# Optimization experiments

Hardware: AMD Instinct MI355X
Metric: run time of the kernel (lower is better)

The kernel has to match this reference:

```python
import jax, jax.numpy as jnp
import numpy as np

BLOCK = 8
NUM_BINS = 64

def _make_dct_basis(n):
    i = np.arange(n)[:, None].astype(np.float64)
    j = np.arange(n)[None, :].astype(np.float64)
    scale = np.where(i == 0, np.sqrt(1.0 / n), np.sqrt(2.0 / n))
    basis = scale * np.cos(np.pi * i * (2.0 * j + 1.0) / (2.0 * n))
    return jnp.asarray(basis, dtype=jnp.float32)

def setup_inputs() -> dict:
    key = jax.random.key(0)
    x = jax.random.normal(key, (32, 3, 512, 512), dtype=jnp.float32)
    return {"x": x, "dct_basis": _make_dct_basis(BLOCK)}

def reference(x, dct_basis):
    B, C, H, W = x.shape
    bs = BLOCK
    # H, W assumed multiples of bs (pad branch is a no-op for these shapes)
    # tile into non-overlapping bs x bs blocks: [B, C, n_blocks, bs, bs]
    blocks = x.reshape(B, C, H // bs, bs, W // bs, bs)
    blocks = blocks.transpose(0, 1, 2, 4, 3, 5).reshape(B, C, -1, bs, bs)
    # 2D block DCT: D @ block @ D^T
    dct = jnp.einsum('ij,bcnjk,kl->bcnil', dct_basis, blocks, dct_basis)
    # flatten coeffs per block, drop DC coefficient
    flat = dct.reshape(B, C, -1, bs * bs)[..., 1:]
    mag = jnp.abs(flat)
    hist_max = jnp.max(mag) * 1.1  # global max, matches torch code
    # torch.histc semantics: uniform bins on [0, hist_max], edge value -> last bin
    bin_idx = jnp.floor(mag * (NUM_BINS / hist_max)).astype(jnp.int32)
    bin_idx = jnp.clip(bin_idx, 0, NUM_BINS - 1)
    # fused per-(b, c) histogram via a single segment_sum
    bc = jnp.arange(B)[:, None] * C + jnp.arange(C)[None, :]  # [B, C]
    seg = (bc[:, :, None, None] * NUM_BINS + bin_idx).reshape(-1)
    counts = jax.ops.segment_sum(
        jnp.ones(seg.shape, dtype=x.dtype), seg, num_segments=B * C * NUM_BINS)
    hists = counts.reshape(B, C * NUM_BINS) / (H * W)
    return hists
```

## Files before the change

### kernel.cpp

```cpp
#include <hip/hip_runtime.h>


#define NUM_BINS 64
#define HREP 16
#define NWG1 1536
#define MAGS_OFF 8192

typedef unsigned int uint;
typedef __fp16 fp16x2 __attribute__((ext_vector_type(2)));

__device__ __forceinline__ void load_block(const float* __restrict__ p, float* blk) {
    #pragma unroll
    for (int r = 0; r < 8; ++r) {
        float4 a = *reinterpret_cast<const float4*>(p + (size_t)r * 512);
        float4 b = *reinterpret_cast<const float4*>(p + (size_t)r * 512 + 4);
        blk[r*8+0]=a.x; blk[r*8+1]=a.y; blk[r*8+2]=a.z; blk[r*8+3]=a.w;
        blk[r*8+4]=b.x; blk[r*8+5]=b.y; blk[r*8+6]=b.z; blk[r*8+7]=b.w;
    }
}

template <typename F>
__device__ __forceinline__ float dct_block_sym(const float* Dh, float* blk, F&& emit) {
    #pragma unroll
    for (int j = 0; j < 4; ++j)
        #pragma unroll
        for (int k = 0; k < 8; ++k) {
            float a = blk[j*8+k], b = blk[(7-j)*8+k];
            blk[j*8+k]     = a + b;
            blk[(7-j)*8+k] = a - b;
        }

    float m = 0.0f;
    #pragma unroll
    for (int i = 0; i < 8; ++i) {
        float u[8];
        #pragma unroll
        for (int k = 0; k < 8; ++k) {
            float s = 0.0f;
            #pragma unroll
            for (int j = 0; j < 4; ++j) {
                int row = (i & 1) ? (7 - j) : j;
                s = fmaf(Dh[i*4+j], blk[row*8+k], s);
            }
            u[k] = s;
        }
        #pragma unroll
        for (int l = 0; l < 4; ++l) {
            float e = 0.0f, o = 0.0f;
            #pragma unroll
            for (int k = 0; k < 4; ++k) {
                e = fmaf(u[2*k],   Dh[(2*k)*4+l],   e);
                o = fmaf(u[2*k+1], Dh[(2*k+1)*4+l], o);
            }
            float v0 = e + o;
            float v1 = e - o;
            float m1 = fabsf(v1);
            m = fmaxf(m, m1);
            emit(m1);
            if (i != 0 || l != 0) {
                float m0 = fabsf(v0);
                m = fmaxf(m, m0);
                emit(m0);
            }
        }
    }
    return m;
}

struct NoEmit { __device__ void operator()(float) const {} };

template <bool WRITE_MAGS>
__global__ __launch_bounds__(256) void dct_max_kernel(
    const float* __restrict__ x, const float* __restrict__ basis,
    float* __restrict__ wgmax, uint* __restrict__ mags, float* __restrict__ out)
{
    __shared__ float wred[4];
    float Dh[32];
    #pragma unroll
    for (int r = 0; r < 8; ++r)
        #pragma unroll
        for (int c = 0; c < 4; ++c)
            Dh[r*4+c] = basis[r*8+c];

    if (blockIdx.x < 24) out[blockIdx.x * 256 + threadIdx.x] = 0.0f;

    int tid = blockIdx.x * 256 + threadIdx.x;
    int bc  = tid >> 12;
    int n   = tid & 4095;
    int hb  = n >> 6, wb = n & 63;
    const float* p = x + ((size_t)bc << 18) + ((size_t)(hb * 8) << 9) + (size_t)(wb * 8);

    float blk[64];
    load_block(p, blk);

    float m;
    if (WRITE_MAGS) {
        uint* wbase = mags + (size_t)(tid >> 6) * 2048 + (tid & 63);
        float flo = 0.0f;
        int   e   = 0;
        m = dct_block_sym(Dh, blk, [&](float mag) {
            if ((e & 1) == 0) {
                flo = mag;
            } else {
                fp16x2 h2 = __builtin_amdgcn_cvt_pkrtz(flo, mag);
                wbase[(e >> 1) * 64] = __builtin_bit_cast(uint, h2);
            }
            ++e;
        });
        fp16x2 h2 = __builtin_amdgcn_cvt_pkrtz(flo, -__builtin_inff());
        wbase[31 * 64] = __builtin_bit_cast(uint, h2);
    } else {
        m = dct_block_sym(Dh, blk, NoEmit{});
    }

    #pragma unroll
    for (int off = 32; off > 0; off >>= 1)
        m = fmaxf(m, __shfl_down(m, off, 64));
    if ((threadIdx.x & 63) == 0) wred[threadIdx.x >> 6] = m;
    __syncthreads();
    if (threadIdx.x == 0)
        wgmax[blockIdx.x] = fmaxf(fmaxf(wred[0], wred[1]), fmaxf(wred[2], wred[3]));
}

__device__ __forceinline__ float reduce_scale(const float* __restrict__ wgmax,
                                              float* wred, float* s_scale) {
    float m = 0.0f;
    for (int i = threadIdx.x; i < NWG1; i += 256) m = fmaxf(m, wgmax[i]);
    #pragma unroll
    for (int off = 32; off > 0; off >>= 1)
        m = fmaxf(m, __shfl_down(m, off, 64));
    if ((threadIdx.x & 63) == 0) wred[threadIdx.x >> 6] = m;
    __syncthreads();
    if (threadIdx.x == 0) {
        float mm = fmaxf(fmaxf(wred[0], wred[1]), fmaxf(wred[2], wred[3]));
        *s_scale = (float)NUM_BINS / (mm * 1.1f);
    }
    __syncthreads();
    return *s_scale;
}

__global__ __launch_bounds__(256) void dct_hist_frommags(
    const uint* __restrict__ mags, const float* __restrict__ wgmax,
    float* __restrict__ out)
{
    __shared__ uint hist[NUM_BINS * HREP];
    __shared__ float wred[4];
    __shared__ float s_scale;
    for (int i = threadIdx.x; i < NUM_BINS * HREP; i += 256) hist[i] = 0;

    float scale = reduce_scale(wgmax, wred, &s_scale);
    int   sub   = threadIdx.x & (HREP - 1);
    int   bc    = blockIdx.x >> 4;

    const uint* src = mags + (size_t)blockIdx.x * 8192 + threadIdx.x * 4;
    #pragma unroll
    for (int j = 0; j < 8; ++j) {
        uint4 v = *reinterpret_cast<const uint4*>(src + (size_t)j * 1024);
        uint w[4] = {v.x, v.y, v.z, v.w};
        #pragma unroll
        for (int u = 0; u < 4; ++u) {
            fp16x2 h2 = __builtin_bit_cast(fp16x2, w[u]);
            float f0 = (float)h2[0];
            float f1 = (float)h2[1];
            int b0 = min((int)(fmaxf(f0, 0.0f) * scale), NUM_BINS - 1);
            int b1 = min((int)(fmaxf(f1, 0.0f) * scale), NUM_BINS - 1);
            if (f0 >= 0.0f) atomicAdd(&hist[b0 * HREP + sub], 1u);
            if (f1 >= 0.0f) atomicAdd(&hist[b1 * HREP + sub], 1u);
        }
    }
    __syncthreads();

    if (threadIdx.x < NUM_BINS) {
        uint c = 0;
        #pragma unroll
        for (int r = 0; r < HREP; ++r) c += hist[threadIdx.x * HREP + r];
        atomicAdd(&out[bc * NUM_BINS + threadIdx.x], (float)c * (1.0f / 262144.0f));
    }
}

__global__ __launch_bounds__(256) void dct_hist_recompute(
    const float* __restrict__ x, const float* __restrict__ basis,
    const float* __restrict__ wgmax, float* __restrict__ out)
{
    __shared__ uint hist[NUM_BINS * HREP];
    __shared__ float wred[4];
    __shared__ float s_scale;
    float Dh[32];
    #pragma unroll
    for (int r = 0; r < 8; ++r)
        #pragma unroll
        for (int c = 0; c < 4; ++c)
            Dh[r*4+c] = basis[r*8+c];
    for (int i = threadIdx.x; i < NUM_BINS * HREP; i += 256) hist[i] = 0;

    float scale = reduce_scale(wgmax, wred, &s_scale);
    int   sub   = threadIdx.x & (HREP - 1);
    int   bc    = blockIdx.x >> 4;
    int   n     = (blockIdx.x & 15) * 256 + threadIdx.x;
    int   hb    = n >> 6, wb = n & 63;
    const float* p = x + ((size_t)bc << 18) + ((size_t)(hb * 8) << 9) + (size_t)(wb * 8);

    float blk[64];
    load_block(p, blk);
    dct_block_sym(Dh, blk, [&](float mag) {
        int bin = min((int)(mag * scale), NUM_BINS - 1);
        atomicAdd(&hist[bin * HREP + sub], 1u);
    });
    __syncthreads();

    if (threadIdx.x < NUM_BINS) {
        uint c = 0;
        #pragma unroll
        for (int r = 0; r < HREP; ++r) c += hist[threadIdx.x * HREP + r];
        atomicAdd(&out[bc * NUM_BINS + threadIdx.x], (float)c * (1.0f / 262144.0f));
    }
}

extern "C" void kernel_launch(void* const* d_in, const int* in_sizes, int n_in,
                              void* d_out, int out_size, void* d_ws, size_t ws_size,
                              hipStream_t stream) {
    const float* x     = (const float*)d_in[0];
    const float* basis = (const float*)d_in[1];
    float* out         = (float*)d_out;
    float* wgmax       = (float*)d_ws;
    uint*  mags        = (uint*)((char*)d_ws + MAGS_OFF);

    const size_t need = (size_t)MAGS_OFF + (size_t)NWG1 * 256 * 128;
    if (ws_size >= need) {
        dct_max_kernel<true><<<NWG1, 256, 0, stream>>>(x, basis, wgmax, mags, out);
        dct_hist_frommags<<<NWG1, 256, 0, stream>>>(mags, wgmax, out);
    } else {
        dct_max_kernel<false><<<NWG1, 256, 0, stream>>>(x, basis, wgmax, mags, out);
        dct_hist_recompute<<<NWG1, 256, 0, stream>>>(x, basis, wgmax, out);
    }
}
```

Measured before the change: 39.25 us.

## Fuse DCT max and histogram into one cooperative kernel with on-chip magnitudes

Replaces the two-kernel pipeline with a single cooperative-launch kernel. Each workgroup computes DCT magnitudes for two 8x8 blocks per thread, keeping one set in shared memory and the other in registers, then uses a grid-wide sync to get the global max before binning. This removes the global write and read-back of the fp16 magnitude buffer and one kernel launch. In exchange it requires 768 co-resident workgroups, which limits occupancy and adds heavy register and LDS pressure, and it falls back to the old path if the cooperative launch fails.

```diff
diff --git a/kernel.cpp b/kernel.cpp
--- a/kernel.cpp
+++ b/kernel.cpp
@@ -1,8 +1,12 @@
 #include <hip/hip_runtime.h>
+#include <hip/hip_cooperative_groups.h>
+
+namespace cg = cooperative_groups;
 
 
 #define NUM_BINS 64
 #define HREP 16
+#define NWGF 768
 #define NWG1 1536
 #define MAGS_OFF 8192
 
@@ -69,6 +73,142 @@
 
 struct NoEmit { __device__ void operator()(float) const {} };
 
+__device__ __forceinline__ float wave_then_wg_max(float m, float* wred) {
+    #pragma unroll
+    for (int off = 32; off > 0; off >>= 1)
+        m = fmaxf(m, __shfl_down(m, off, 64));
+    if ((threadIdx.x & 63) == 0) wred[threadIdx.x >> 6] = m;
+    __syncthreads();
+    return fmaxf(fmaxf(wred[0], wred[1]), fmaxf(wred[2], wred[3]));
+}
+
+__global__ __launch_bounds__(256, 3) void dct_fused(
+    const float* __restrict__ x, const float* __restrict__ basis,
+    float* __restrict__ wgmax, float* __restrict__ out)
+{
+    __shared__ uint  magsL[256 * 32];
+    __shared__ uint  hist[NUM_BINS * HREP];
+    __shared__ float wred[4];
+    __shared__ float s_scale;
+
+    float Dh[32];
+    #pragma unroll
+    for (int r = 0; r < 8; ++r)
+        #pragma unroll
+        for (int c = 0; c < 4; ++c)
+            Dh[r*4+c] = basis[r*8+c];
+
+    for (int i = threadIdx.x; i < NUM_BINS * HREP; i += 256) hist[i] = 0;
+    if (blockIdx.x < 24) out[blockIdx.x * 256 + threadIdx.x] = 0.0f;
+
+    const int base = blockIdx.x * 512;
+    float m = 0.0f;
+
+    {
+        int bi = base + threadIdx.x;
+        int bc = bi >> 12, n = bi & 4095;
+        const float* p = x + ((size_t)bc << 18) + ((size_t)((n >> 6) * 8) << 9)
+                           + (size_t)((n & 63) * 8);
+        float blk[64];
+        load_block(p, blk);
+        uint* myL = magsL + threadIdx.x;
+        float flo = 0.0f;
+        int   e   = 0;
+        m = dct_block_sym(Dh, blk, [&](float mag) {
+            if ((e & 1) == 0) flo = mag;
+            else {
+                fp16x2 h2 = __builtin_amdgcn_cvt_pkrtz(flo, mag);
+                myL[(e >> 1) * 256] = __builtin_bit_cast(uint, h2);
+            }
+            ++e;
+        });
+        fp16x2 h2 = __builtin_amdgcn_cvt_pkrtz(flo, 0.0f);
+        myL[31 * 256] = __builtin_bit_cast(uint, h2);
+    }
+
+    uint magR[32];
+    {
+        int bi = base + 256 + threadIdx.x;
+        int bc = bi >> 12, n = bi & 4095;
+        const float* p = x + ((size_t)bc << 18) + ((size_t)((n >> 6) * 8) << 9)
+                           + (size_t)((n & 63) * 8);
+        float blk[64];
+        load_block(p, blk);
+        float flo = 0.0f;
+        int   e   = 0;
+        float m2 = dct_block_sym(Dh, blk, [&](float mag) {
+            if ((e & 1) == 0) flo = mag;
+            else {
+                fp16x2 h2 = __builtin_amdgcn_cvt_pkrtz(flo, mag);
+                magR[e >> 1] = __builtin_bit_cast(uint, h2);
+            }
+            ++e;
+        });
+        fp16x2 h2 = __builtin_amdgcn_cvt_pkrtz(flo, 0.0f);
+        magR[31] = __builtin_bit_cast(uint, h2);
+        m = fmaxf(m, m2);
+    }
+
+    float wm = wave_then_wg_max(m, wred);
+    if (threadIdx.x == 0) wgmax[blockIdx.x] = wm;
+
+    cg::this_grid().sync();
+
+    {
+        float g = fmaxf(fmaxf(wgmax[threadIdx.x],       wgmax[threadIdx.x + 256]),
+                        wgmax[threadIdx.x + 512]);
+        #pragma unroll
+        for (int off = 32; off > 0; off >>= 1)
+            g = fmaxf(g, __shfl_down(g, off, 64));
+        if ((threadIdx.x & 63) == 0) wred[threadIdx.x >> 6] = g;
+        __syncthreads();
+        if (threadIdx.x == 0) {
+            float mm = fmaxf(fmaxf(wred[0], wred[1]), fmaxf(wred[2], wred[3]));
+            s_scale = (float)NUM_BINS / (mm * 1.1f);
+        }
+        __syncthreads();
+    }
+    float scale = s_scale;
+    int   sub   = threadIdx.x & (HREP - 1);
+
+    #pragma unroll
+    for (int q = 0; q < 32; ++q) {
+        fp16x2 h2 = __builtin_bit_cast(fp16x2, magR[q]);
+        float f0 = (float)h2[0];
+        int b0 = min((int)(f0 * scale), NUM_BINS - 1);
+        atomicAdd(&hist[b0 * HREP + sub], 1u);
+        if (q < 31) {
+            float f1 = (float)h2[1];
+            int b1 = min((int)(f1 * scale), NUM_BINS - 1);
+            atomicAdd(&hist[b1 * HREP + sub], 1u);
+        }
+    }
+    {
+        const uint* myL = magsL + threadIdx.x;
+        #pragma unroll
+        for (int q = 0; q < 32; ++q) {
+            fp16x2 h2 = __builtin_bit_cast(fp16x2, myL[q * 256]);
+            float f0 = (float)h2[0];
+            int b0 = min((int)(f0 * scale), NUM_BINS - 1);
+            atomicAdd(&hist[b0 * HREP + sub], 1u);
+            if (q < 31) {
+                float f1 = (float)h2[1];
+                int b1 = min((int)(f1 * scale), NUM_BINS - 1);
+                atomicAdd(&hist[b1 * HREP + sub], 1u);
+            }
+        }
+    }
+    __syncthreads();
+
+    if (threadIdx.x < NUM_BINS) {
+        uint c = 0;
+        #pragma unroll
+        for (int r = 0; r < HREP; ++r) c += hist[threadIdx.x * HREP + r];
+        int bc = blockIdx.x >> 3;
+        atomicAdd(&out[bc * NUM_BINS + threadIdx.x], (float)c * (1.0f / 262144.0f));
+    }
+}
+
 template <bool WRITE_MAGS>
 __global__ __launch_bounds__(256) void dct_max_kernel(
     const float* __restrict__ x, const float* __restrict__ basis,
@@ -85,11 +225,9 @@
     if (blockIdx.x < 24) out[blockIdx.x * 256 + threadIdx.x] = 0.0f;
 
     int tid = blockIdx.x * 256 + threadIdx.x;
-    int bc  = tid >> 12;
-    int n   = tid & 4095;
-    int hb  = n >> 6, wb = n & 63;
-    const float* p = x + ((size_t)bc << 18) + ((size_t)(hb * 8) << 9) + (size_t)(wb * 8);
-
+    int bc  = tid >> 12, n = tid & 4095;
+    const float* p = x + ((size_t)bc << 18) + ((size_t)((n >> 6) * 8) << 9)
+                       + (size_t)((n & 63) * 8);
     float blk[64];
     load_block(p, blk);
 
@@ -99,9 +237,8 @@
         float flo = 0.0f;
         int   e   = 0;
         m = dct_block_sym(Dh, blk, [&](float mag) {
-            if ((e & 1) == 0) {
-                flo = mag;
-            } else {
+            if ((e & 1) == 0) flo = mag;
+            else {
                 fp16x2 h2 = __builtin_amdgcn_cvt_pkrtz(flo, mag);
                 wbase[(e >> 1) * 64] = __builtin_bit_cast(uint, h2);
             }
@@ -113,28 +250,16 @@
         m = dct_block_sym(Dh, blk, NoEmit{});
     }
 
-    #pragma unroll
-    for (int off = 32; off > 0; off >>= 1)
-        m = fmaxf(m, __shfl_down(m, off, 64));
-    if ((threadIdx.x & 63) == 0) wred[threadIdx.x >> 6] = m;
-    __syncthreads();
-    if (threadIdx.x == 0)
-        wgmax[blockIdx.x] = fmaxf(fmaxf(wred[0], wred[1]), fmaxf(wred[2], wred[3]));
+    float wm = wave_then_wg_max(m, wred);
+    if (threadIdx.x == 0) wgmax[blockIdx.x] = wm;
 }
 
 __device__ __forceinline__ float reduce_scale(const float* __restrict__ wgmax,
                                               float* wred, float* s_scale) {
     float m = 0.0f;
     for (int i = threadIdx.x; i < NWG1; i += 256) m = fmaxf(m, wgmax[i]);
-    #pragma unroll
-    for (int off = 32; off > 0; off >>= 1)
-        m = fmaxf(m, __shfl_down(m, off, 64));
-    if ((threadIdx.x & 63) == 0) wred[threadIdx.x >> 6] = m;
-    __syncthreads();
-    if (threadIdx.x == 0) {
-        float mm = fmaxf(fmaxf(wred[0], wred[1]), fmaxf(wred[2], wred[3]));
-        *s_scale = (float)NUM_BINS / (mm * 1.1f);
-    }
+    float wm = wave_then_wg_max(m, wred);
+    if (threadIdx.x == 0) *s_scale = (float)NUM_BINS / (wm * 1.1f);
     __syncthreads();
     return *s_scale;
 }
@@ -197,9 +322,8 @@
     int   sub   = threadIdx.x & (HREP - 1);
     int   bc    = blockIdx.x >> 4;
     int   n     = (blockIdx.x & 15) * 256 + threadIdx.x;
-    int   hb    = n >> 6, wb = n & 63;
-    const float* p = x + ((size_t)bc << 18) + ((size_t)(hb * 8) << 9) + (size_t)(wb * 8);
-
+    const float* p = x + ((size_t)bc << 18) + ((size_t)((n >> 6) * 8) << 9)
+                       + (size_t)((n & 63) * 8);
     float blk[64];
     load_block(p, blk);
     dct_block_sym(Dh, blk, [&](float mag) {
@@ -225,6 +349,12 @@
     float* wgmax       = (float*)d_ws;
     uint*  mags        = (uint*)((char*)d_ws + MAGS_OFF);
 
+    void* args[] = {(void*)&x, (void*)&basis, (void*)&wgmax, (void*)&out};
+    hipError_t err = hipLaunchCooperativeKernel(
+        (const void*)dct_fused, dim3(NWGF), dim3(256), args, 0, stream);
+    if (err == hipSuccess) return;
+    (void)hipGetLastError();
+
     const size_t need = (size_t)MAGS_OFF + (size_t)NWG1 * 256 * 128;
     if (ws_size >= need) {
         dct_max_kernel<true><<<NWG1, 256, 0, stream>>>(x, basis, wgmax, mags, out);
```

After: 111.5 us. 2.84x slower.
